# Kernel optimization log

Measured on AMD Instinct MI355X. Metric: run time of the kernel, lower is better.

Reference implementation:

```python
import jax, jax.numpy as jnp
import numpy as np

HIDDEN = 2048
N_HEADS = 16
HEAD_DIM = HIDDEN // N_HEADS  # 128
GROUP_SIZE = 128
ROPE_THETA = 10000.0
EPS = 1e-8
THRESH = 0.5


def ternary_quantize_groupwise(w):
    O, I = w.shape
    wg = w.reshape(O, I // GROUP_SIZE, GROUP_SIZE)
    scale = jnp.maximum(jnp.mean(jnp.abs(wg), axis=-1, keepdims=True), EPS)
    wn = wg / scale
    q = jnp.where(wn > THRESH, 1.0, jnp.where(wn < -THRESH, -1.0, 0.0))
    return (q * scale).reshape(O, I)


def quantize_with_ste(w):
    wq = ternary_quantize_groupwise(w)
    return w + jax.lax.stop_gradient(wq - w)


def rope_tables(seqlen):
    half = HEAD_DIM // 2
    inv_freq = 1.0 / (ROPE_THETA ** (jnp.arange(half, dtype=jnp.float32) / half))
    freqs = jnp.arange(seqlen, dtype=jnp.float32)[:, None] * inv_freq[None, :]  # [S, half]
    return jnp.cos(freqs), jnp.sin(freqs)


def apply_rope(x, cos, sin):
    # x: [B, H, S, D]; cos/sin: [S, D/2]
    d = x.shape[-1]
    x1, x2 = x[..., : d // 2], x[..., d // 2:]
    c = cos[None, None, :, :].astype(x.dtype)
    s = sin[None, None, :, :].astype(x.dtype)
    return jnp.concatenate([x1 * c - x2 * s, x1 * s + x2 * c], axis=-1)


def setup_inputs() -> dict:
    key = jax.random.key(0)
    ks = jax.random.split(key, 5)
    B, S = 1, 2048
    hidden_states = jax.random.normal(ks[0], (B, S, HIDDEN), dtype=jnp.float32)
    attention_mask = jnp.ones((B, S), dtype=jnp.int32)
    init_scale = 1.0 / np.sqrt(HIDDEN)
    wq = jax.random.normal(ks[1], (HIDDEN, HIDDEN), dtype=jnp.float32) * init_scale
    wk = jax.random.normal(ks[2], (HIDDEN, HIDDEN), dtype=jnp.float32) * init_scale
    wv = jax.random.normal(ks[3], (HIDDEN, HIDDEN), dtype=jnp.float32) * init_scale
    wo = jax.random.normal(ks[4], (HIDDEN, HIDDEN), dtype=jnp.float32) * init_scale
    return {"hidden_states": hidden_states, "attention_mask": attention_mask,
            "wq": wq, "wk": wk, "wv": wv, "wo": wo}


def reference(hidden_states, attention_mask, wq, wk, wv, wo):
    B, S, _ = hidden_states.shape
    cos, sin = rope_tables(S)

    def proj(x, w):
        w_q = quantize_with_ste(w)
        y = jnp.einsum('bsi,oi->bso', x, w_q)
        return y.reshape(B, S, N_HEADS, HEAD_DIM).transpose(0, 2, 1, 3)  # [B,H,S,D]

    q = apply_rope(proj(hidden_states, wq), cos, sin)
    k = apply_rope(proj(hidden_states, wk), cos, sin)
    v = proj(hidden_states, wv)

    scores = jnp.einsum('bhsd,bhtd->bhst', q, k) / np.sqrt(HEAD_DIM)
    causal = jnp.triu(jnp.ones((S, S), dtype=bool), k=1)
    scores = jnp.where(causal[None, None, :, :], -jnp.inf, scores)
    pad = (attention_mask == 0)[:, None, None, :]
    scores = jnp.where(pad, -jnp.inf, scores)

    probs = jax.nn.softmax(scores, axis=-1)
    out = jnp.einsum('bhst,bhtd->bhsd', probs, v)
    out = out.transpose(0, 2, 1, 3).reshape(B, S, HIDDEN)

    wo_q = quantize_with_ste(wo)
    return jnp.einsum('bso,po->bsp', out, wo_q)
```

## Files before the change

kernel.cpp:

```cpp
#include <hip/hip_runtime.h>
#include <cstdint>
#include <cstddef>


typedef __attribute__((ext_vector_type(8))) short bf16x8;
typedef __attribute__((ext_vector_type(4))) float f32x4;
typedef __attribute__((address_space(3))) void lds_void;
typedef const __attribute__((address_space(1))) void gmem_void;

__device__ __forceinline__ short f2bf(float x) {
    union { float f; uint32_t u; } c; c.f = x;
    uint32_t r = (c.u + 0x7FFFu + ((c.u >> 16) & 1u)) >> 16;
    return (short)r;
}
__device__ __forceinline__ float bf2f(short x) {
    union { uint32_t u; float f; } c; c.u = ((uint32_t)(uint16_t)x) << 16;
    return c.f;
}

__global__ __launch_bounds__(64) void zero_flag(int* f) {
    if (threadIdx.x == 0) *f = 0;
}

__global__ __launch_bounds__(256) void detect_kernel(
    const unsigned short* __restrict__ p, int n, int* __restrict__ flag)
{
    int tid = blockIdx.x * 256 + threadIdx.x;
    int cnt = 0;
    for (int i = tid; i < n; i += 65536) {
        int e = (p[i] >> 7) & 0xFF;
        cnt += (e >= 0xF0) ? 1 : 0;
    }
#pragma unroll
    for (int off = 1; off < 64; off <<= 1) cnt += __shfl_xor(cnt, off);
    if ((threadIdx.x & 63) == 0 && cnt) atomicAdd(flag, cnt);
}

__global__ __launch_bounds__(256) void convert_kernel(
    const void* __restrict__ in, short* __restrict__ out, int n,
    const int* __restrict__ flag)
{
    bool isf32 = (*flag > 1000);
    int i = blockIdx.x * 256 + threadIdx.x;
    if (i >= n) return;
    out[i] = isf32 ? f2bf(((const float*)in)[i]) : ((const short*)in)[i];
}

__global__ __launch_bounds__(256) void quant_kernel(
    const void* __restrict__ w0, const void* __restrict__ w1,
    const void* __restrict__ w2, const void* __restrict__ w3,
    short* __restrict__ q0, short* __restrict__ q1,
    short* __restrict__ q2, short* __restrict__ q3,
    const int* __restrict__ flag)
{
    bool isf32 = (*flag > 1000);
    int gw   = blockIdx.x * 4 + (threadIdx.x >> 6);
    int lane = threadIdx.x & 63;
    int mat  = gw >> 15;
    int g    = gw & 32767;
    const void* w = (mat == 0) ? w0 : (mat == 1) ? w1 : (mat == 2) ? w2 : w3;
    short*      q = (mat == 0) ? q0 : (mat == 1) ? q1 : (mat == 2) ? q2 : q3;
    int idx = g * 64 + lane;
    float a, b;
    if (isf32) {
        const float* wf = (const float*)w;
        a = wf[idx * 2]; b = wf[idx * 2 + 1];
    } else {
        int pr = ((const int*)w)[idx];
        a = bf2f((short)(pr & 0xFFFF));
        b = bf2f((short)(((uint32_t)pr) >> 16));
    }
    float s = fabsf(a) + fabsf(b);
#pragma unroll
    for (int off = 1; off < 64; off <<= 1) s += __shfl_xor(s, off);
    float scale = fmaxf(s * (1.0f / 128.0f), 1e-8f);
    float na = a / scale, nb = b / scale;
    float ra = (na > 0.5f) ? scale : (na < -0.5f) ? -scale : 0.0f;
    float rb = (nb > 0.5f) ? scale : (nb < -0.5f) ? -scale : 0.0f;
    ((int*)q)[idx] = (int)(uint16_t)f2bf(ra) | ((int)(uint16_t)f2bf(rb) << 16);
}

template<int OM, bool CSKIP, bool CK>
__global__ __launch_bounds__(256) void gemm_bt(
    const short* __restrict__ A, const short* __restrict__ B, void* __restrict__ C,
    int M, int N, int K, int lda, int ldb, int ldc, float scale,
    long long sA, long long sB, long long sC)
{
    int bx = blockIdx.x, by = blockIdx.y, bz = blockIdx.z;
    if (CSKIP && bx > by) return;
    const short* Ab = A + (long long)bz * sA + (long long)by * 128 * lda;
    const short* Bb = B + (long long)bz * sB + (long long)bx * 128 * ldb;
    __shared__ short lA[128 * 64];
    __shared__ short lB[128 * 64];
    int tid = threadIdx.x;
    int lane = tid & 63, wv = tid >> 6;
    int Kend = K;
    if (CK) { int kl = (by + 1) * 128; Kend = kl < K ? kl : K; }
    f32x4 acc[4][4];
#pragma unroll
    for (int i = 0; i < 4; i++)
#pragma unroll
        for (int j = 0; j < 4; j++)
#pragma unroll
            for (int r = 0; r < 4; r++) acc[i][j][r] = 0.0f;

    int rbase = (wv >> 1) * 64, cbase = (wv & 1) * 64;

    for (int k0 = 0; k0 < Kend; k0 += 64) {
        __syncthreads();
#pragma unroll
        for (int i = 0; i < 4; i++) {
            int ci  = i * 256 + tid;
            int row = ci >> 3;
            int kcG = (ci & 7) ^ (row & 7);
            const short* gp = Ab + (long long)row * lda + k0 + kcG * 8;
            __builtin_amdgcn_global_load_lds((gmem_void*)gp, (lds_void*)(lA + ci * 8), 16, 0, 0);
        }
#pragma unroll
        for (int i = 0; i < 4; i++) {
            int ci  = i * 256 + tid;
            int row = ci >> 3;
            int kcG = (ci & 7) ^ (row & 7);
            const short* gp = Bb + (long long)row * ldb + k0 + kcG * 8;
            __builtin_amdgcn_global_load_lds((gmem_void*)gp, (lds_void*)(lB + ci * 8), 16, 0, 0);
        }
        __syncthreads();
#pragma unroll
        for (int kk = 0; kk < 2; kk++) {
            int kc = kk * 4 + (lane >> 4);
            bf16x8 a[4], b[4];
#pragma unroll
            for (int t = 0; t < 4; t++) {
                int r = rbase + t * 16 + (lane & 15);
                a[t] = *(const bf16x8*)(lA + (r * 8 + (kc ^ (r & 7))) * 8);
            }
#pragma unroll
            for (int t = 0; t < 4; t++) {
                int r = cbase + t * 16 + (lane & 15);
                b[t] = *(const bf16x8*)(lB + (r * 8 + (kc ^ (r & 7))) * 8);
            }
#pragma unroll
            for (int mt = 0; mt < 4; mt++)
#pragma unroll
                for (int nt = 0; nt < 4; nt++)
                    acc[mt][nt] = __builtin_amdgcn_mfma_f32_16x16x32_bf16(a[mt], b[nt], acc[mt][nt], 0, 0, 0);
        }
    }

    int rq = (lane >> 4) * 4, cq = lane & 15;
#pragma unroll
    for (int mt = 0; mt < 4; mt++) {
#pragma unroll
        for (int nt = 0; nt < 4; nt++) {
#pragma unroll
            for (int r = 0; r < 4; r++) {
                int row = by * 128 + rbase + mt * 16 + rq + r;
                int col = bx * 128 + cbase + nt * 16 + cq;
                float v = acc[mt][nt][r] * scale;
                if (OM == 0) {
                    float* Cp = (float*)C + (long long)bz * sC;
                    Cp[(long long)row * ldc + col] = v;
                } else if (OM == 1) {
                    short* Cp = (short*)C + (long long)bz * sC;
                    Cp[(long long)row * ldc + col] = f2bf(v);
                } else {
                    short* Cp = (short*)C + (long long)bz * sC;
                    Cp[(long long)col * ldc + row] = f2bf(v);
                }
            }
        }
    }
}

__global__ __launch_bounds__(256) void rope_kernel(
    const float* __restrict__ qkv,
    short* __restrict__ qr, short* __restrict__ kr)
{
    int idx = blockIdx.x * 256 + threadIdx.x;
    int d = idx & 63;
    int h = (idx >> 6) & 15;
    int s = idx >> 10;
    float inv = exp2f((float)d * -0.20762050593261719f);
    float ang = (float)s * inv;
    float sn, c;
    sincosf(ang, &sn, &c);
    long long io = (long long)s * 6144 + h * 128 + d;
    long long oo = (long long)h * 262144 + (long long)s * 128 + d;
    float x1 = qkv[io], x2 = qkv[io + 64];
    qr[oo]      = f2bf(x1 * c - x2 * sn);
    qr[oo + 64] = f2bf(x1 * sn + x2 * c);
    x1 = qkv[io + 2048]; x2 = qkv[io + 2112];
    kr[oo]      = f2bf(x1 * c - x2 * sn);
    kr[oo + 64] = f2bf(x1 * sn + x2 * c);
}

__global__ __launch_bounds__(256) void vtrans_kernel(
    const float* __restrict__ qkv, short* __restrict__ v_t)
{
    int ot = blockIdx.x, tt = blockIdx.y;
    __shared__ short lt[64][72];
    int tid = threadIdx.x;
    int tr = tid >> 4, tc = tid & 15;
#pragma unroll
    for (int i = 0; i < 4; i++) {
        int t = tr + i * 16;
        const float* gp = qkv + (long long)(tt * 64 + t) * 6144 + 4096 + ot * 64 + tc * 4;
        float4 v = *(const float4*)gp;
        lt[tc * 4 + 0][t] = f2bf(v.x);
        lt[tc * 4 + 1][t] = f2bf(v.y);
        lt[tc * 4 + 2][t] = f2bf(v.z);
        lt[tc * 4 + 3][t] = f2bf(v.w);
    }
    __syncthreads();
    int orr = tid >> 3, oc = tid & 7;
#pragma unroll
    for (int i = 0; i < 2; i++) {
        int o = orr + i * 32;
        bf16x8 val = *(const bf16x8*)(&lt[o][oc * 8]);
        *(bf16x8*)(v_t + (long long)(ot * 64 + o) * 2048 + tt * 64 + oc * 8) = val;
    }
}

__global__ __launch_bounds__(256) void flash_kernel(
    const short* __restrict__ q_r, const short* __restrict__ k_r,
    const short* __restrict__ v_t, float* __restrict__ Opart,
    float* __restrict__ mpart, float* __restrict__ lpart)
{
    const float SC = 0.08838834764831845f;
    int bid = blockIdx.x;
    int qt = 31 - (bid >> 5);
    int h  = (bid >> 1) & 15;
    int z  = bid & 1;
    int n  = qt + 1;
    int jhalf = (n + 1) >> 1;
    int jb = z ? jhalf : 0;
    int je = z ? n : jhalf;

    int tid = threadIdx.x, lane = tid & 63, wv = tid >> 6;
    int quad = lane >> 4, lm = lane & 15;

    __shared__ short lK[64 * 128];
    __shared__ short lV[128 * 64];
    __shared__ short lP[64 * 64];

    const short* qb = q_r + h * 262144 + (qt * 64 + wv * 16) * 128;
    const short* kb = k_r + h * 262144;
    const short* vb = v_t + h * 128 * 2048;

    bf16x8 aq[4];
#pragma unroll
    for (int kc = 0; kc < 4; kc++)
        aq[kc] = *(const bf16x8*)(qb + lm * 128 + kc * 32 + quad * 8);

    f32x4 ao[8];
#pragma unroll
    for (int nt = 0; nt < 8; nt++)
#pragma unroll
        for (int r = 0; r < 4; r++) ao[nt][r] = 0.0f;
    float mrow[4], lrow[4];
#pragma unroll
    for (int r = 0; r < 4; r++) { mrow[r] = -1e30f; lrow[r] = 0.0f; }

    if (jb < je) {
#pragma unroll
        for (int i = 0; i < 4; i++) {
            int ci = i * 256 + tid;
            int r = ci >> 4, cp = ci & 15;
            int c = (cp & 8) | ((cp & 7) ^ (r & 7));
            const short* gp = kb + (jb * 64 + r) * 128 + c * 8;
            __builtin_amdgcn_global_load_lds((gmem_void*)gp, (lds_void*)(lK + ci * 8), 16, 0, 0);
        }
    }
    __syncthreads();

    for (int jt = jb; jt < je; jt++) {
#pragma unroll
        for (int i = 0; i < 4; i++) {
            int ci = i * 256 + tid;
            int r = ci >> 3, cp = ci & 7;
            int c = cp ^ (r & 7);
            const short* gp = vb + r * 2048 + jt * 64 + c * 8;
            __builtin_amdgcn_global_load_lds((gmem_void*)gp, (lds_void*)(lV + ci * 8), 16, 0, 0);
        }
        f32x4 as[4];
#pragma unroll
        for (int nt = 0; nt < 4; nt++)
#pragma unroll
            for (int r = 0; r < 4; r++) as[nt][r] = 0.0f;
#pragma unroll
        for (int kc = 0; kc < 4; kc++) {
#pragma unroll
            for (int nt = 0; nt < 4; nt++) {
                int r = nt * 16 + lm;
                int c = kc * 4 + quad;
                int slot = (c & 8) | ((c & 7) ^ (r & 7));
                bf16x8 bk = *(const bf16x8*)(lK + (r * 16 + slot) * 8);
                as[nt] = __builtin_amdgcn_mfma_f32_16x16x32_bf16(aq[kc], bk, as[nt], 0, 0, 0);
            }
        }
        bool diag = (jt == qt);
#pragma unroll
        for (int nt = 0; nt < 4; nt++)
#pragma unroll
            for (int r = 0; r < 4; r++) {
                float s = as[nt][r] * SC;
                if (diag) {
                    int qg = wv * 16 + quad * 4 + r;
                    int tg = nt * 16 + lm;
                    if (tg > qg) s = -1e30f;
                }
                as[nt][r] = s;
            }
#pragma unroll
        for (int r = 0; r < 4; r++) {
            float mx = fmaxf(fmaxf(as[0][r], as[1][r]), fmaxf(as[2][r], as[3][r]));
#pragma unroll
            for (int off = 1; off < 16; off <<= 1) mx = fmaxf(mx, __shfl_xor(mx, off));
            float mnew = fmaxf(mrow[r], mx);
            float alpha = __expf(mrow[r] - mnew);
            mrow[r] = mnew;
            float psum = 0.0f;
#pragma unroll
            for (int nt = 0; nt < 4; nt++) {
                float p = __expf(as[nt][r] - mnew);
                as[nt][r] = p;
                psum += p;
            }
#pragma unroll
            for (int off = 1; off < 16; off <<= 1) psum += __shfl_xor(psum, off);
            lrow[r] = lrow[r] * alpha + psum;
#pragma unroll
            for (int nt = 0; nt < 8; nt++) ao[nt][r] *= alpha;
            int row = wv * 16 + quad * 4 + r;
#pragma unroll
            for (int nt = 0; nt < 4; nt++) {
                int slot = (nt * 2 + (lm >> 3) + row) & 7;
                lP[row * 64 + slot * 8 + (lm & 7)] = f2bf(as[nt][r]);
            }
        }
        __syncthreads();
        if (jt + 1 < je) {
#pragma unroll
            for (int i = 0; i < 4; i++) {
                int ci = i * 256 + tid;
                int r = ci >> 4, cp = ci & 15;
                int c = (cp & 8) | ((cp & 7) ^ (r & 7));
                const short* gp = kb + ((jt + 1) * 64 + r) * 128 + c * 8;
                __builtin_amdgcn_global_load_lds((gmem_void*)gp, (lds_void*)(lK + ci * 8), 16, 0, 0);
            }
        }
#pragma unroll
        for (int kt = 0; kt < 2; kt++) {
            int prow = wv * 16 + lm;
            int slot = (kt * 4 + quad + prow) & 7;
            bf16x8 ap = *(const bf16x8*)(lP + prow * 64 + slot * 8);
#pragma unroll
            for (int nt = 0; nt < 8; nt++) {
                int r = nt * 16 + lm;
                int c = kt * 4 + quad;
                int vslot = c ^ (r & 7);
                bf16x8 bv = *(const bf16x8*)(lV + (r * 8 + vslot) * 8);
                ao[nt] = __builtin_amdgcn_mfma_f32_16x16x32_bf16(ap, bv, ao[nt], 0, 0, 0);
            }
        }
        __syncthreads();
    }
    float* Ob = Opart + (long long)z * 4194304;
#pragma unroll
    for (int r = 0; r < 4; r++) {
        int sg = qt * 64 + wv * 16 + quad * 4 + r;
#pragma unroll
        for (int nt = 0; nt < 8; nt++) {
            int dg = h * 128 + nt * 16 + lm;
            Ob[(long long)sg * 2048 + dg] = ao[nt][r];
        }
        if (lm == 0) {
            mpart[z * 32768 + h * 2048 + sg] = mrow[r];
            lpart[z * 32768 + h * 2048 + sg] = lrow[r];
        }
    }
}

__global__ __launch_bounds__(256) void combine_kernel(
    const float* __restrict__ O0, const float* __restrict__ O1,
    const float* __restrict__ mpart, const float* __restrict__ lpart,
    short* __restrict__ attn)
{
    int idx = blockIdx.x * 256 + threadIdx.x;
    int e = idx * 4;
    int s = e >> 11, h = (e & 2047) >> 7;
    float m0 = mpart[h * 2048 + s], m1 = mpart[32768 + h * 2048 + s];
    float l0 = lpart[h * 2048 + s], l1 = lpart[32768 + h * 2048 + s];
    float M = fmaxf(m0, m1);
    float w0 = __expf(m0 - M), w1 = __expf(m1 - M);
    float inv = 1.0f / (l0 * w0 + l1 * w1);
    float4 a = *(const float4*)(O0 + e);
    float4 b = *(const float4*)(O1 + e);
    short4 o;
    o.x = f2bf((a.x * w0 + b.x * w1) * inv);
    o.y = f2bf((a.y * w0 + b.y * w1) * inv);
    o.z = f2bf((a.z * w0 + b.z * w1) * inv);
    o.w = f2bf((a.w * w0 + b.w * w1) * inv);
    *(short4*)(attn + e) = o;
}

extern "C" void kernel_launch(void* const* d_in, const int* in_sizes, int n_in,
                              void* d_out, int out_size, void* d_ws, size_t ws_size,
                              hipStream_t stream)
{
    const void* x  = d_in[0];
    const void* wq = d_in[2];
    const void* wk = d_in[3];
    const void* wv = d_in[4];
    const void* wo = d_in[5];

    char* ws = (char*)d_ws;
    size_t off = 0;
    auto alloc = [&](size_t b) { void* p = ws + off; off += (b + 255) & ~(size_t)255; return p; };
    short* wqkv_q = (short*)alloc(25165824);
    short* wo_q   = (short*)alloc(8388608);
    float* qkv    = (float*)alloc(50331648);
    short* v_t    = (short*)alloc(8388608);
    short* q_r    = (short*)alloc(8388608);
    short* k_r    = (short*)alloc(8388608);
    short* attn   = (short*)alloc(8388608);
    short* x_bf   = (short*)alloc(8388608);
    float* Opart  = (float*)alloc(33554432);
    float* mpart  = (float*)alloc(262144);
    float* lpart  = (float*)alloc(262144);
    int*   flag   = (int*)alloc(256);
    if (off > ws_size) return;

    zero_flag<<<1, 64, 0, stream>>>(flag);
    detect_kernel<<<256, 256, 0, stream>>>(
        (const unsigned short*)x, in_sizes[0], flag);
    convert_kernel<<<16384, 256, 0, stream>>>(x, x_bf, 4194304, flag);

    quant_kernel<<<32768, 256, 0, stream>>>(wq, wk, wv, wo,
        wqkv_q, wqkv_q + 4194304, wqkv_q + 8388608, wo_q, flag);

    gemm_bt<0,false,false><<<dim3(48,16,1), 256, 0, stream>>>(
        x_bf, wqkv_q, qkv, 2048,6144,2048, 2048,2048,6144, 1.0f, 0,0,0);

    rope_kernel<<<8192, 256, 0, stream>>>(qkv, q_r, k_r);
    vtrans_kernel<<<dim3(32,32), 256, 0, stream>>>(qkv, v_t);

    flash_kernel<<<1024, 256, 0, stream>>>(q_r, k_r, v_t, Opart, mpart, lpart);
    combine_kernel<<<4096, 256, 0, stream>>>(
        Opart, Opart + 4194304, mpart, lpart, attn);

    gemm_bt<0,false,false><<<dim3(16,16,1), 256, 0, stream>>>(
        attn, wo_q, d_out, 2048,2048,2048, 2048,2048,2048, 1.0f, 0,0,0);
}
```

Before: 334.1 us.

## Fuse V transpose into QKV GEMM epilogue, emit bf16, retile output GEMM

The QKV projection GEMM now writes Q/K as bf16 and writes V directly transposed in bf16, which removes the separate vtrans kernel and the large fp32 qkv intermediate. The rope kernel reads bf16 input. The output projection gets a dedicated kernel with 128x64 tiles, doubling the block count from 256 to 512 to fill more CUs. Trade-offs: Q/K are rounded to bf16 before RoPE, a small accuracy change, and the transposed V stores are strided and uncoalesced.

Measured after the change: 333.9 us. Within noise of the previous version (-0.1%).

```diff
diff --git a/kernel.cpp b/kernel.cpp
--- a/kernel.cpp
+++ b/kernel.cpp
@@ -80,22 +80,17 @@
     ((int*)q)[idx] = (int)(uint16_t)f2bf(ra) | ((int)(uint16_t)f2bf(rb) << 16);
 }
 
-template<int OM, bool CSKIP, bool CK>
-__global__ __launch_bounds__(256) void gemm_bt(
-    const short* __restrict__ A, const short* __restrict__ B, void* __restrict__ C,
-    int M, int N, int K, int lda, int ldb, int ldc, float scale,
-    long long sA, long long sB, long long sC)
-{
-    int bx = blockIdx.x, by = blockIdx.y, bz = blockIdx.z;
-    if (CSKIP && bx > by) return;
-    const short* Ab = A + (long long)bz * sA + (long long)by * 128 * lda;
-    const short* Bb = B + (long long)bz * sB + (long long)bx * 128 * ldb;
+__global__ __launch_bounds__(256) void gemm_qkv(
+    const short* __restrict__ A, const short* __restrict__ B,
+    short* __restrict__ Cqk, short* __restrict__ Cv)
+{
+    int bx = blockIdx.x, by = blockIdx.y;
+    const short* Ab = A + (long long)by * 128 * 2048;
+    const short* Bb = B + (long long)bx * 128 * 2048;
     __shared__ short lA[128 * 64];
     __shared__ short lB[128 * 64];
     int tid = threadIdx.x;
     int lane = tid & 63, wv = tid >> 6;
-    int Kend = K;
-    if (CK) { int kl = (by + 1) * 128; Kend = kl < K ? kl : K; }
     f32x4 acc[4][4];
 #pragma unroll
     for (int i = 0; i < 4; i++)
@@ -106,14 +101,14 @@
 
     int rbase = (wv >> 1) * 64, cbase = (wv & 1) * 64;
 
-    for (int k0 = 0; k0 < Kend; k0 += 64) {
+    for (int k0 = 0; k0 < 2048; k0 += 64) {
         __syncthreads();
 #pragma unroll
         for (int i = 0; i < 4; i++) {
             int ci  = i * 256 + tid;
             int row = ci >> 3;
             int kcG = (ci & 7) ^ (row & 7);
-            const short* gp = Ab + (long long)row * lda + k0 + kcG * 8;
+            const short* gp = Ab + (long long)row * 2048 + k0 + kcG * 8;
             __builtin_amdgcn_global_load_lds((gmem_void*)gp, (lds_void*)(lA + ci * 8), 16, 0, 0);
         }
 #pragma unroll
@@ -121,7 +116,7 @@
             int ci  = i * 256 + tid;
             int row = ci >> 3;
             int kcG = (ci & 7) ^ (row & 7);
-            const short* gp = Bb + (long long)row * ldb + k0 + kcG * 8;
+            const short* gp = Bb + (long long)row * 2048 + k0 + kcG * 8;
             __builtin_amdgcn_global_load_lds((gmem_void*)gp, (lds_void*)(lB + ci * 8), 16, 0, 0);
         }
         __syncthreads();
@@ -148,32 +143,108 @@
     }
 
     int rq = (lane >> 4) * 4, cq = lane & 15;
-#pragma unroll
-    for (int mt = 0; mt < 4; mt++) {
-#pragma unroll
-        for (int nt = 0; nt < 4; nt++) {
+    if (bx < 32) {
+#pragma unroll
+        for (int mt = 0; mt < 4; mt++)
+#pragma unroll
+            for (int nt = 0; nt < 4; nt++)
+#pragma unroll
+                for (int r = 0; r < 4; r++) {
+                    int row = by * 128 + rbase + mt * 16 + rq + r;
+                    int col = bx * 128 + cbase + nt * 16 + cq;
+                    Cqk[(long long)row * 4096 + col] = f2bf(acc[mt][nt][r]);
+                }
+    } else {
+#pragma unroll
+        for (int mt = 0; mt < 4; mt++)
+#pragma unroll
+            for (int nt = 0; nt < 4; nt++)
+#pragma unroll
+                for (int r = 0; r < 4; r++) {
+                    int row = by * 128 + rbase + mt * 16 + rq + r;
+                    int colv = (bx - 32) * 128 + cbase + nt * 16 + cq;
+                    Cv[(long long)colv * 2048 + row] = f2bf(acc[mt][nt][r]);
+                }
+    }
+}
+
+__global__ __launch_bounds__(256) void gemm_wo(
+    const short* __restrict__ A, const short* __restrict__ B,
+    float* __restrict__ C)
+{
+    int bx = blockIdx.x, by = blockIdx.y;
+    const short* Ab = A + (long long)by * 128 * 2048;
+    const short* Bb = B + (long long)bx * 64 * 2048;
+    __shared__ short lA[128 * 64];
+    __shared__ short lB[64 * 64];
+    int tid = threadIdx.x;
+    int lane = tid & 63, wv = tid >> 6;
+    f32x4 acc[2][4];
+#pragma unroll
+    for (int i = 0; i < 2; i++)
+#pragma unroll
+        for (int j = 0; j < 4; j++)
+#pragma unroll
+            for (int r = 0; r < 4; r++) acc[i][j][r] = 0.0f;
+
+    int rbase = wv * 32;
+
+    for (int k0 = 0; k0 < 2048; k0 += 64) {
+        __syncthreads();
+#pragma unroll
+        for (int i = 0; i < 4; i++) {
+            int ci  = i * 256 + tid;
+            int row = ci >> 3;
+            int kcG = (ci & 7) ^ (row & 7);
+            const short* gp = Ab + (long long)row * 2048 + k0 + kcG * 8;
+            __builtin_amdgcn_global_load_lds((gmem_void*)gp, (lds_void*)(lA + ci * 8), 16, 0, 0);
+        }
+#pragma unroll
+        for (int i = 0; i < 2; i++) {
+            int ci  = i * 256 + tid;
+            int row = ci >> 3;
+            int kcG = (ci & 7) ^ (row & 7);
+            const short* gp = Bb + (long long)row * 2048 + k0 + kcG * 8;
+            __builtin_amdgcn_global_load_lds((gmem_void*)gp, (lds_void*)(lB + ci * 8), 16, 0, 0);
+        }
+        __syncthreads();
+#pragma unroll
+        for (int kk = 0; kk < 2; kk++) {
+            int kc = kk * 4 + (lane >> 4);
+            bf16x8 a[2], b[4];
+#pragma unroll
+            for (int t = 0; t < 2; t++) {
+                int r = rbase + t * 16 + (lane & 15);
+                a[t] = *(const bf16x8*)(lA + (r * 8 + (kc ^ (r & 7))) * 8);
+            }
+#pragma unroll
+            for (int t = 0; t < 4; t++) {
+                int r = t * 16 + (lane & 15);
+                b[t] = *(const bf16x8*)(lB + (r * 8 + (kc ^ (r & 7))) * 8);
+            }
+#pragma unroll
+            for (int mt = 0; mt < 2; mt++)
+#pragma unroll
+                for (int nt = 0; nt < 4; nt++)
+                    acc[mt][nt] = __builtin_amdgcn_mfma_f32_16x16x32_bf16(a[mt], b[nt], acc[mt][nt], 0, 0, 0);
+        }
+    }
+
+    int rq = (lane >> 4) * 4, cq = lane & 15;
+#pragma unroll
+    for (int mt = 0; mt < 2; mt++)
+#pragma unroll
+        for (int nt = 0; nt < 4; nt++)
 #pragma unroll
             for (int r = 0; r < 4; r++) {
                 int row = by * 128 + rbase + mt * 16 + rq + r;
-                int col = bx * 128 + cbase + nt * 16 + cq;
-                float v = acc[mt][nt][r] * scale;
-                if (OM == 0) {
-                    float* Cp = (float*)C + (long long)bz * sC;
-                    Cp[(long long)row * ldc + col] = v;
-                } else if (OM == 1) {
-                    short* Cp = (short*)C + (long long)bz * sC;
-                    Cp[(long long)row * ldc + col] = f2bf(v);
-                } else {
-                    short* Cp = (short*)C + (long long)bz * sC;
-                    Cp[(long long)col * ldc + row] = f2bf(v);
-                }
-            }
-        }
-    }
+                int col = bx * 64 + nt * 16 + cq;
+                C[(long long)row * 2048 + col] = acc[mt][nt][r];
+            }
 }
 
 __global__ __launch_bounds__(256) void rope_kernel(
-    const float* __restrict__ qkv,
+    const short* __restrict__ qk,
     short* __restrict__ qr, short* __restrict__ kr)
 {
     int idx = blockIdx.x * 256 + threadIdx.x;
@@ -184,41 +255,14 @@
     float ang = (float)s * inv;
     float sn, c;
     sincosf(ang, &sn, &c);
-    long long io = (long long)s * 6144 + h * 128 + d;
+    long long io = (long long)s * 4096 + h * 128 + d;
     long long oo = (long long)h * 262144 + (long long)s * 128 + d;
-    float x1 = qkv[io], x2 = qkv[io + 64];
+    float x1 = bf2f(qk[io]), x2 = bf2f(qk[io + 64]);
     qr[oo]      = f2bf(x1 * c - x2 * sn);
     qr[oo + 64] = f2bf(x1 * sn + x2 * c);
-    x1 = qkv[io + 2048]; x2 = qkv[io + 2112];
+    x1 = bf2f(qk[io + 2048]); x2 = bf2f(qk[io + 2112]);
     kr[oo]      = f2bf(x1 * c - x2 * sn);
     kr[oo + 64] = f2bf(x1 * sn + x2 * c);
-}
-
-__global__ __launch_bounds__(256) void vtrans_kernel(
-    const float* __restrict__ qkv, short* __restrict__ v_t)
-{
-    int ot = blockIdx.x, tt = blockIdx.y;
-    __shared__ short lt[64][72];
-    int tid = threadIdx.x;
-    int tr = tid >> 4, tc = tid & 15;
-#pragma unroll
-    for (int i = 0; i < 4; i++) {
-        int t = tr + i * 16;
-        const float* gp = qkv + (long long)(tt * 64 + t) * 6144 + 4096 + ot * 64 + tc * 4;
-        float4 v = *(const float4*)gp;
-        lt[tc * 4 + 0][t] = f2bf(v.x);
-        lt[tc * 4 + 1][t] = f2bf(v.y);
-        lt[tc * 4 + 2][t] = f2bf(v.z);
-        lt[tc * 4 + 3][t] = f2bf(v.w);
-    }
-    __syncthreads();
-    int orr = tid >> 3, oc = tid & 7;
-#pragma unroll
-    for (int i = 0; i < 2; i++) {
-        int o = orr + i * 32;
-        bf16x8 val = *(const bf16x8*)(&lt[o][oc * 8]);
-        *(bf16x8*)(v_t + (long long)(ot * 64 + o) * 2048 + tt * 64 + oc * 8) = val;
-    }
 }
 
 __global__ __launch_bounds__(256) void flash_kernel(
@@ -419,7 +463,7 @@
     auto alloc = [&](size_t b) { void* p = ws + off; off += (b + 255) & ~(size_t)255; return p; };
     short* wqkv_q = (short*)alloc(25165824);
     short* wo_q   = (short*)alloc(8388608);
-    float* qkv    = (float*)alloc(50331648);
+    short* qk     = (short*)alloc(16777216);
     short* v_t    = (short*)alloc(8388608);
     short* q_r    = (short*)alloc(8388608);
     short* k_r    = (short*)alloc(8388608);
@@ -439,16 +483,13 @@
     quant_kernel<<<32768, 256, 0, stream>>>(wq, wk, wv, wo,
         wqkv_q, wqkv_q + 4194304, wqkv_q + 8388608, wo_q, flag);
 
-    gemm_bt<0,false,false><<<dim3(48,16,1), 256, 0, stream>>>(
-        x_bf, wqkv_q, qkv, 2048,6144,2048, 2048,2048,6144, 1.0f, 0,0,0);
-
-    rope_kernel<<<8192, 256, 0, stream>>>(qkv, q_r, k_r);
-    vtrans_kernel<<<dim3(32,32), 256, 0, stream>>>(qkv, v_t);
+    gemm_qkv<<<dim3(48,16), 256, 0, stream>>>(x_bf, wqkv_q, qk, v_t);
+
+    rope_kernel<<<8192, 256, 0, stream>>>(qk, q_r, k_r);
 
     flash_kernel<<<1024, 256, 0, stream>>>(q_r, k_r, v_t, Opart, mpart, lpart);
     combine_kernel<<<4096, 256, 0, stream>>>(
         Opart, Opart + 4194304, mpart, lpart, attn);
 
-    gemm_bt<0,false,false><<<dim3(16,16,1), 256, 0, stream>>>(
-        attn, wo_q, d_out, 2048,2048,2048, 2048,2048,2048, 1.0f, 0,0,0);
-}
+    gemm_wo<<<dim3(32,16), 256, 0, stream>>>(attn, wo_q, (float*)d_out);
+}
```
